# Kernel tuning notes

Hardware: AMD Instinct MI355X
Metric: run time of the kernel (lower is better)

## Reference

```python
import jax, jax.numpy as jnp
import numpy as np

N, E, D, ED, G = 50000, 800000, 64, 32, 50


def setup_inputs() -> dict:
    key = jax.random.key(0)
    ks = jax.random.split(key, 24)
    s = 0.05
    inp = {
        "x": jax.random.normal(ks[0], (N, D), jnp.float32),
        "edge_attr": jax.random.normal(ks[1], (E, ED), jnp.float32),
        "edge_index": jax.random.randint(ks[2], (2, E), 0, N, jnp.int64),
    }
    i = 3
    for step in range(2):
        inp[f"fe{step}_W1"] = jax.random.normal(ks[i], (2 * D + ED, D), jnp.float32) * s; i += 1
        inp[f"fe{step}_b1"] = jnp.zeros((D,), jnp.float32)
        inp[f"fe{step}_W2"] = jax.random.normal(ks[i], (D, D), jnp.float32) * s; i += 1
        inp[f"fe{step}_b2"] = jnp.zeros((D,), jnp.float32)
        inp[f"lstm{step}_Wih"] = jax.random.normal(ks[i], (D, 4 * D), jnp.float32) * s; i += 1
        inp[f"lstm{step}_Whh"] = jax.random.normal(ks[i], (D, 4 * D), jnp.float32) * s; i += 1
        inp[f"lstm{step}_bih"] = jnp.zeros((4 * D,), jnp.float32)
        inp[f"lstm{step}_bhh"] = jnp.zeros((4 * D,), jnp.float32)
    inp["gm_W"] = jax.random.normal(ks[i], (D, G), jnp.float32) * s; i += 1
    inp["gm_b"] = jnp.zeros((G,), jnp.float32)
    inp["fm_W"] = jax.random.normal(ks[i], (D, G), jnp.float32) * s; i += 1
    inp["fm_b"] = jnp.zeros((G,), jnp.float32)
    return inp


def _mpn(x, edge_attr, src, dst, W1, b1, W2, b2):
    # x_i = x[dst] (target), x_j = x[src] (source); aggregate 'add' at dst
    m = jnp.concatenate([x[dst], x[src], edge_attr], axis=1)  # [E, 2D+ED]
    m = jax.nn.relu(m @ W1 + b1) @ W2 + b2                    # [E, D]
    return jax.ops.segment_sum(m, dst, num_segments=x.shape[0])


def _lstm_cell(inp, h, c, Wih, Whh, bih, bhh):
    gates = inp @ Wih + h @ Whh + (bih + bhh)  # [N, 4D], gate order i,f,g,o
    i, f, g, o = jnp.split(gates, 4, axis=1)
    c = jax.nn.sigmoid(f) * c + jax.nn.sigmoid(i) * jnp.tanh(g)
    h = jax.nn.sigmoid(o) * jnp.tanh(c)
    return h, c


def reference(x, edge_attr, edge_index,
              fe0_W1, fe0_b1, fe0_W2, fe0_b2,
              lstm0_Wih, lstm0_Whh, lstm0_bih, lstm0_bhh,
              fe1_W1, fe1_b1, fe1_W2, fe1_b2,
              lstm1_Wih, lstm1_Whh, lstm1_bih, lstm1_bhh,
              gm_W, gm_b, fm_W, fm_b):
    src, dst = edge_index[0], edge_index[1]
    c = jnp.zeros_like(x)
    fes = [(fe0_W1, fe0_b1, fe0_W2, fe0_b2), (fe1_W1, fe1_b1, fe1_W2, fe1_b2)]
    lstms = [(lstm0_Wih, lstm0_Whh, lstm0_bih, lstm0_bhh),
             (lstm1_Wih, lstm1_Whh, lstm1_bih, lstm1_bhh)]
    for step in range(2):
        a = _mpn(x, edge_attr, src, dst, *fes[step])
        # LSTMCell(input=x, (h=a, c=c)) as in the original forward
        x, c = _lstm_cell(x, a, c, *lstms[step])
    g = jax.nn.sigmoid(x @ gm_W + gm_b)   # [N, G]
    h_v_G = x @ fm_W + fm_b               # [N, G]
    return jnp.sum(g * h_v_G, axis=0)     # [G]
```

## Files before the change

### kernel.cpp

```cpp
#include <hip/hip_runtime.h>
#include <hip/hip_bf16.h>

using short8 = __attribute__((ext_vector_type(8))) short;
using f32x4  = __attribute__((ext_vector_type(4))) float;

#define K1P 168
#define KLP 136

__device__ __forceinline__ unsigned short f2bf(float f) {
  unsigned u = __float_as_uint(f);
  u += 0x7FFFu + ((u >> 16) & 1u);
  return (unsigned short)(u >> 16);
}
__device__ __forceinline__ unsigned pack2(float a, float b) {
  return (unsigned)f2bf(a) | ((unsigned)f2bf(b) << 16);
}
#if __has_builtin(__builtin_amdgcn_rcpf)
__device__ __forceinline__ float fast_rcp(float x) { return __builtin_amdgcn_rcpf(x); }
#else
__device__ __forceinline__ float fast_rcp(float x) { return 1.f / x; }
#endif
__device__ __forceinline__ float sigm(float x) { return fast_rcp(1.f + __expf(-x)); }
__device__ __forceinline__ float tanh_f(float x) { return fmaf(2.f, sigm(2.f * x), -1.f); }

__global__ __launch_bounds__(256) void prep_simple(
    const float* __restrict__ W1_0, const float* __restrict__ Wih0,
    const float* __restrict__ bih0, const float* __restrict__ bhh0,
    const float* __restrict__ W1_1, const float* __restrict__ Wih1,
    const float* __restrict__ bih1, const float* __restrict__ bhh1,
    const float* __restrict__ gmW, const float* __restrict__ fmW,
    unsigned short* __restrict__ W1T,
    unsigned short* __restrict__ WcT,
    float* __restrict__ bG,
    unsigned short* __restrict__ WrT)
{
  int t = blockIdx.x * 256 + threadIdx.x;
  const int per = 10240 + 16384 + 256;
  if (t >= 2 * per + 8192) return;
  if (t >= 2 * per) {
    int r2 = t - 2 * per;
    int o = r2 >> 6, k = r2 & 63;
    float v = 0.f;
    if (o < 50) v = gmW[k * 50 + o];
    else if (o >= 64 && o < 114) v = fmW[k * 50 + (o - 64)];
    WrT[o * 64 + k] = f2bf(v);
    return;
  }
  int step = t / per, r = t % per;
  const float* W1  = step ? W1_1 : W1_0;
  const float* Wih = step ? Wih1 : Wih0;
  const float* bih = step ? bih1 : bih0;
  const float* bhh = step ? bhh1 : bhh0;
  if (r < 10240) {
    int o = r / 160, k = r % 160;
    W1T[step * 10240 + o * 160 + k] = f2bf(W1[k * 64 + o]);
  } else if (r < 26624) {
    int rr = r - 10240;
    int g = rr >> 6, k = rr & 63;
    WcT[step * 32768 + g * 128 + k] = f2bf(Wih[k * 256 + g]);
  } else {
    int g = r - 26624;
    bG[step * 256 + g] = bih[g] + bhh[g];
  }
}

__global__ __launch_bounds__(256) void prep_merge(
    const float* __restrict__ W2_0, const float* __restrict__ Whh0, const float* __restrict__ b2_0,
    const float* __restrict__ W2_1, const float* __restrict__ Whh1, const float* __restrict__ b2_1,
    unsigned short* __restrict__ WcT,
    float* __restrict__ b2h)
{
  int t = blockIdx.x * 256 + threadIdx.x;
  if (t < 32768) {
    int step = t >> 14, r = t & 16383;
    int g = r >> 6, k = r & 63;
    const float* W2  = step ? W2_1 : W2_0;
    const float* Whh = step ? Whh1 : Whh0;
    float v = 0.f;
    for (int j = 0; j < 64; ++j) v = fmaf(W2[k * 64 + j], Whh[j * 256 + g], v);
    WcT[step * 32768 + g * 128 + 64 + k] = f2bf(v);
  } else if (t < 33280) {
    int r = t - 32768;
    int step = r >> 8, g = r & 255;
    const float* b2  = step ? b2_1 : b2_0;
    const float* Whh = step ? Whh1 : Whh0;
    float v = 0.f;
    for (int j = 0; j < 64; ++j) v = fmaf(b2[j], Whh[j * 256 + g], v);
    b2h[step * 256 + g] = v;
  }
}

__global__ __launch_bounds__(256) void convert_x(
    const float* __restrict__ x, unsigned short* __restrict__ xb, int n)
{
  int i = blockIdx.x * 256 + threadIdx.x;
  if (i < n) xb[i] = f2bf(x[i]);
}

__global__ __launch_bounds__(256) void hist_kernel(
    const int* __restrict__ dstI, int* __restrict__ hist, int E)
{
  int e = blockIdx.x * 256 + threadIdx.x;
  if (e < E) atomicAdd(&hist[dstI[e]], 1);
}

__global__ __launch_bounds__(256) void scan_part(
    const int* __restrict__ hist, int2* __restrict__ blockTot, int N)
{
  __shared__ int sD[256], sS[256];
  int t = threadIdx.x;
  int n = blockIdx.x * 256 + t;
  int d = (n < N) ? hist[n] : 0;
  int sg = (d + 15) >> 4;
  sD[t] = d; sS[t] = sg;
  __syncthreads();
  #pragma unroll
  for (int off = 128; off; off >>= 1) {
    if (t < off) { sD[t] += sD[t + off]; sS[t] += sS[t + off]; }
    __syncthreads();
  }
  if (t == 0) blockTot[blockIdx.x] = make_int2(sD[0], sS[0]);
}

__global__ __launch_bounds__(256) void scan_mid(
    const int2* __restrict__ blockTot, int2* __restrict__ blockBase,
    int* __restrict__ nSegTot, int nb)
{
  __shared__ int sD[256], sS[256];
  int t = threadIdx.x;
  int d = 0, s = 0;
  if (t < nb) { int2 v = blockTot[t]; d = v.x; s = v.y; }
  sD[t] = d; sS[t] = s;
  __syncthreads();
  #pragma unroll
  for (int off = 1; off < 256; off <<= 1) {
    int vd = (t >= off) ? sD[t - off] : 0;
    int vs = (t >= off) ? sS[t - off] : 0;
    __syncthreads();
    sD[t] += vd; sS[t] += vs;
    __syncthreads();
  }
  if (t < nb) blockBase[t] = make_int2(sD[t] - d, sS[t] - s);
  if (t == nb - 1) *nSegTot = sS[t];
}

__global__ __launch_bounds__(256) void scan_final(
    const int* __restrict__ hist, const int2* __restrict__ blockBase,
    int* __restrict__ cursor, int4* __restrict__ segInfo, int N)
{
  __shared__ int sD[256], sS[256];
  int t = threadIdx.x;
  int n = blockIdx.x * 256 + t;
  int d = (n < N) ? hist[n] : 0;
  int sg = (d + 15) >> 4;
  sD[t] = d; sS[t] = sg;
  __syncthreads();
  #pragma unroll
  for (int off = 1; off < 256; off <<= 1) {
    int vd = (t >= off) ? sD[t - off] : 0;
    int vs = (t >= off) ? sS[t - off] : 0;
    __syncthreads();
    sD[t] += vd; sS[t] += vs;
    __syncthreads();
  }
  if (n < N) {
    int2 bb = blockBase[blockIdx.x];
    int degBase = bb.x + sD[t] - d;
    int segBase = bb.y + sS[t] - sg;
    cursor[n] = degBase;
    for (int j = 0; j < sg; ++j)
      segInfo[segBase + j] = make_int4(degBase + j * 16, n, min(d - j * 16, 16), 0);
  }
}

__global__ __launch_bounds__(256) void scatter_perm(
    const int* __restrict__ srcI, const int* __restrict__ dstI,
    const float* __restrict__ ea, int* __restrict__ cursor,
    int* __restrict__ srcS, unsigned short* __restrict__ eaS, int E)
{
  int e = blockIdx.x * 256 + threadIdx.x;
  if (e >= E) return;
  int d = dstI[e];
  int p = atomicAdd(&cursor[d], 1);
  srcS[p] = srcI[e];
  const float4* pe = (const float4*)(ea + (long long)e * 32);
  float4 a0 = pe[0], a1 = pe[1], a2 = pe[2], a3 = pe[3];
  float4 a4 = pe[4], a5 = pe[5], a6 = pe[6], a7 = pe[7];
  uint4* out = (uint4*)(eaS + (long long)p * 32);
  out[0] = make_uint4(pack2(a0.x, a0.y), pack2(a0.z, a0.w), pack2(a1.x, a1.y), pack2(a1.z, a1.w));
  out[1] = make_uint4(pack2(a2.x, a2.y), pack2(a2.z, a2.w), pack2(a3.x, a3.y), pack2(a3.z, a3.w));
  out[2] = make_uint4(pack2(a4.x, a4.y), pack2(a4.z, a4.w), pack2(a5.x, a5.y), pack2(a5.z, a5.w));
  out[3] = make_uint4(pack2(a6.x, a6.y), pack2(a6.z, a6.w), pack2(a7.x, a7.y), pack2(a7.z, a7.w));
}

__global__ __launch_bounds__(256) void edge_gemm_agg(
    const unsigned short* __restrict__ xb,
    const unsigned short* __restrict__ eaS,
    const int* __restrict__ srcS,
    const int4* __restrict__ segInfo,
    const int* __restrict__ nSegPtr,
    const unsigned short* __restrict__ W1T,
    const float* __restrict__ b1,
    float* __restrict__ aggrH)
{
  __shared__ unsigned short sM[64 * K1P];
  __shared__ unsigned short sW1[64 * 21 * 8];
  __shared__ float sB1[64];
  const int t = threadIdx.x;
  {
    const uint4* gw1 = (const uint4*)W1T;
    uint4* lw1 = (uint4*)sW1;
    #pragma unroll
    for (int p = 0; p < 5; ++p) {
      int idx = t + p * 256;
      int o = idx / 20, s = idx % 20;
      lw1[o * 21 + s] = gw1[idx];
    }
    if (t < 64) sB1[t] = b1[t];
  }
  __syncthreads();

  const int w = t >> 6, l = t & 63;
  const int quad = l >> 4, lr = l & 15;
  const int r = l >> 2, q = l & 3;
  unsigned short* rowp = sM + (w * 16 + r) * K1P;
  const int nSeg = *nSegPtr;
  const int W = gridDim.x * 4;

  for (int s = blockIdx.x * 4 + w; s < nSeg; s += W) {
    int4 si = segInfo[s];
    const int start = si.x, node = si.y, cnt = si.z;

    const uint4* pd = (const uint4*)(xb + (long long)node * 64);
    *(uint4*)(rowp + q * 16)     = pd[q * 2];
    *(uint4*)(rowp + q * 16 + 8) = pd[q * 2 + 1];
    int src = (r < cnt) ? srcS[start + r] : 0;
    const uint4* ps = (const uint4*)(xb + (long long)src * 64);
    *(uint4*)(rowp + 64 + q * 16)     = ps[q * 2];
    *(uint4*)(rowp + 64 + q * 16 + 8) = ps[q * 2 + 1];
    const uint4* pe = (const uint4*)(eaS + (long long)(start + r) * 32);
    *(uint4*)(rowp + 128 + q * 8) = pe[q];

    f32x4 acc[4] = {};
    #pragma unroll
    for (int kc = 0; kc < 5; ++kc) {
      short8 aF = *(const short8*)(sM + (w * 16 + lr) * K1P + kc * 32 + quad * 8);
      #pragma unroll
      for (int n = 0; n < 4; ++n) {
        short8 bF = *(const short8*)(sW1 + (n * 16 + lr) * K1P + kc * 32 + quad * 8);
        acc[n] = __builtin_amdgcn_mfma_f32_16x16x32_bf16(aF, bF, acc[n], 0, 0, 0);
      }
    }

    #pragma unroll
    for (int n = 0; n < 4; ++n) {
      int col = n * 16 + lr;
      float bb = sB1[col];
      float sum = 0.f;
      #pragma unroll
      for (int rr = 0; rr < 4; ++rr) {
        int rowi = quad * 4 + rr;
        float v = fmaxf(acc[n][rr] + bb, 0.f);
        sum += (rowi < cnt) ? v : 0.f;
      }
      sum += __shfl_xor(sum, 16);
      sum += __shfl_xor(sum, 32);
      if (quad == 0) unsafeAtomicAdd(&aggrH[(long long)node * 64 + col], sum);
    }
  }
}

__global__ __launch_bounds__(256) void lstm3(
    const float* __restrict__ xin,
    const float* __restrict__ aggrH,
    const float* __restrict__ cin,
    float* __restrict__ cout,
    const unsigned short* __restrict__ WcT,
    const float* __restrict__ bG,
    const float* __restrict__ b2h,
    const int* __restrict__ degA,
    float* __restrict__ xout,
    unsigned short* __restrict__ xbf_out,
    int nNodes)
{
  __shared__ unsigned short sIn[64 * KLP];
  __shared__ unsigned short sW[64 * KLP];
  __shared__ float sBG[256], sB2h[256];
  const int t = threadIdx.x;
  sBG[t] = bG[t];
  sB2h[t] = b2h[t];

  const int base_n = blockIdx.x * 64;
  const int nl = t >> 2, q = t & 3;
  const int node = base_n + nl;
  unsigned short* rowp = sIn + nl * KLP;
  if (node < nNodes) {
    const float4* px = (const float4*)(xin + (long long)node * 64) + q * 4;
    float4 v0 = px[0], v1 = px[1], v2 = px[2], v3 = px[3];
    *(uint4*)(rowp + q * 16) =
        make_uint4(pack2(v0.x, v0.y), pack2(v0.z, v0.w), pack2(v1.x, v1.y), pack2(v1.z, v1.w));
    *(uint4*)(rowp + q * 16 + 8) =
        make_uint4(pack2(v2.x, v2.y), pack2(v2.z, v2.w), pack2(v3.x, v3.y), pack2(v3.z, v3.w));
    const float4* pg = (const float4*)(aggrH + (long long)node * 64) + q * 4;
    float4 g0 = pg[0], g1 = pg[1], g2 = pg[2], g3 = pg[3];
    *(uint4*)(rowp + 64 + q * 16) =
        make_uint4(pack2(g0.x, g0.y), pack2(g0.z, g0.w), pack2(g1.x, g1.y), pack2(g1.z, g1.w));
    *(uint4*)(rowp + 64 + q * 16 + 8) =
        make_uint4(pack2(g2.x, g2.y), pack2(g2.z, g2.w), pack2(g3.x, g3.y), pack2(g3.z, g3.w));
  } else {
    *(uint4*)(rowp + q * 16)          = make_uint4(0, 0, 0, 0);
    *(uint4*)(rowp + q * 16 + 8)      = make_uint4(0, 0, 0, 0);
    *(uint4*)(rowp + 64 + q * 16)     = make_uint4(0, 0, 0, 0);
    *(uint4*)(rowp + 64 + q * 16 + 8) = make_uint4(0, 0, 0, 0);
  }

  const int w = t >> 6, l = t & 63, quad = l >> 4, lr = l & 15;
  const int row0 = w * 16;
  f32x4 acc[16] = {};
  for (int grp = 0; grp < 4; ++grp) {
    const uint4* gw = (const uint4*)WcT + (long long)(grp * 64) * 16;
    uint4* lw = (uint4*)sW;
    {
      int o0 = t >> 4, s4 = t & 15;
      #pragma unroll
      for (int p = 0; p < 4; ++p) {
        int o = p * 16 + o0;
        lw[o * 17 + s4] = gw[o * 16 + s4];
      }
    }
    __syncthreads();
    #pragma unroll
    for (int kc = 0; kc < 4; ++kc) {
      short8 aF = *(const short8*)(sIn + (row0 + lr) * KLP + kc * 32 + quad * 8);
      #pragma unroll
      for (int nt = 0; nt < 4; ++nt) {
        short8 bF = *(const short8*)(sW + (nt * 16 + lr) * KLP + kc * 32 + quad * 8);
        acc[grp * 4 + nt] = __builtin_amdgcn_mfma_f32_16x16x32_bf16(aF, bF, acc[grp * 4 + nt], 0, 0, 0);
      }
    }
    __syncthreads();
  }

  #pragma unroll
  for (int nt = 0; nt < 4; ++nt) {
    #pragma unroll
    for (int rr = 0; rr < 4; ++rr) {
      int node2 = base_n + row0 + quad * 4 + rr;
      if (node2 < nNodes) {
        int col = nt * 16 + lr;
        long long off = (long long)node2 * 64 + col;
        float dg = (float)degA[node2];
        float iv = acc[nt][rr]      + sBG[col]       + dg * sB2h[col];
        float fv = acc[4 + nt][rr]  + sBG[64 + col]  + dg * sB2h[64 + col];
        float gv = acc[8 + nt][rr]  + sBG[128 + col] + dg * sB2h[128 + col];
        float ov = acc[12 + nt][rr] + sBG[192 + col] + dg * sB2h[192 + col];
        float cOld = cin ? cin[off] : 0.f;
        float cN = sigm(fv) * cOld + sigm(iv) * tanh_f(gv);
        float hN = sigm(ov) * tanh_f(cN);
        cout[off] = cN;
        xout[off] = hN;
        if (xbf_out) xbf_out[off] = f2bf(hN);
      }
    }
  }
}

__global__ __launch_bounds__(256) void readout(
    const float* __restrict__ x,
    const unsigned short* __restrict__ WrT,
    const float* __restrict__ gb, const float* __restrict__ fb,
    float* __restrict__ out, int nNodes)
{
  __shared__ unsigned short sX[64 * 72];
  __shared__ unsigned short sW[128 * 72];
  __shared__ float sOut[4][64];
  __shared__ float sGb[64], sFb[64];
  const int t = threadIdx.x;
  {
    const uint4* gw = (const uint4*)WrT;
    uint4* lw = (uint4*)sW;
    #pragma unroll
    for (int p = 0; p < 4; ++p) {
      int idx = t + p * 256;
      int o = idx >> 3, s = idx & 7;
      lw[o * 9 + s] = gw[idx];
    }
    if (t < 50)      { sGb[t] = gb[t]; sFb[t] = fb[t]; }
    else if (t < 64) { sGb[t] = 0.f;   sFb[t] = 0.f; }
  }
  const int base = blockIdx.x * 64;
  const int nl = t >> 2, q = t & 3;
  const int node = base + nl;
  {
    uint2* dst = (uint2*)(sX + nl * 72 + q * 16);
    if (node < nNodes) {
      const float4* px = (const float4*)(x + (long long)node * 64) + q * 4;
      #pragma unroll
      for (int j = 0; j < 4; ++j) {
        float4 v = px[j];
        dst[j] = make_uint2(pack2(v.x, v.y), pack2(v.z, v.w));
      }
    } else {
      #pragma unroll
      for (int j = 0; j < 4; ++j) dst[j] = make_uint2(0, 0);
    }
  }
  __syncthreads();

  const int w = t >> 6, l = t & 63, quad = l >> 4, lr = l & 15;
  f32x4 acc[8] = {};
  #pragma unroll
  for (int kc = 0; kc < 2; ++kc) {
    short8 aF = *(const short8*)(sX + (w * 16 + lr) * 72 + kc * 32 + quad * 8);
    #pragma unroll
    for (int n = 0; n < 8; ++n) {
      short8 bF = *(const short8*)(sW + (n * 16 + lr) * 72 + kc * 32 + quad * 8);
      acc[n] = __builtin_amdgcn_mfma_f32_16x16x32_bf16(aF, bF, acc[n], 0, 0, 0);
    }
  }
  #pragma unroll
  for (int n = 0; n < 4; ++n) {
    float val = 0.f;
    #pragma unroll
    for (int rr = 0; rr < 4; ++rr) {
      int nd = base + w * 16 + quad * 4 + rr;
      if (nd < nNodes) {
        int jj = n * 16 + lr;
        float gv = sigm(acc[n][rr] + sGb[jj]);
        float fv = acc[n + 4][rr] + sFb[jj];
        val += gv * fv;
      }
    }
    val += __shfl_xor(val, 16);
    val += __shfl_xor(val, 32);
    if (quad == 0) sOut[w][n * 16 + lr] = val;
  }
  __syncthreads();
  if (t < 50) {
    float s = sOut[0][t] + sOut[1][t] + sOut[2][t] + sOut[3][t];
    unsafeAtomicAdd(&out[t], s);
  }
}

extern "C" void kernel_launch(void* const* d_in, const int* in_sizes, int n_in,
                              void* d_out, int out_size, void* d_ws, size_t ws_size,
                              hipStream_t stream)
{
  const float* x      = (const float*)d_in[0];
  const float* ea     = (const float*)d_in[1];
  const int*   ei     = (const int*)d_in[2];
  const float* fe0_W1 = (const float*)d_in[3];
  const float* fe0_b1 = (const float*)d_in[4];
  const float* fe0_W2 = (const float*)d_in[5];
  const float* fe0_b2 = (const float*)d_in[6];
  const float* l0_Wih = (const float*)d_in[7];
  const float* l0_Whh = (const float*)d_in[8];
  const float* l0_bih = (const float*)d_in[9];
  const float* l0_bhh = (const float*)d_in[10];
  const float* fe1_W1 = (const float*)d_in[11];
  const float* fe1_b1 = (const float*)d_in[12];
  const float* fe1_W2 = (const float*)d_in[13];
  const float* fe1_b2 = (const float*)d_in[14];
  const float* l1_Wih = (const float*)d_in[15];
  const float* l1_Whh = (const float*)d_in[16];
  const float* l1_bih = (const float*)d_in[17];
  const float* l1_bhh = (const float*)d_in[18];
  const float* gm_W   = (const float*)d_in[19];
  const float* gm_b   = (const float*)d_in[20];
  const float* fm_W   = (const float*)d_in[21];
  const float* fm_b   = (const float*)d_in[22];

  const int N = in_sizes[0] / 64;
  const int E = in_sizes[1] / 32;
  const int* srcI = ei;
  const int* dstI = ei + E;

  char* ws = (char*)d_ws;
  unsigned short* xb      = (unsigned short*)(ws + 0);
  float*          x1      = (float*)(ws + 6400000);
  float*          aggrH   = (float*)(ws + 19200000);
  float*          cbuf    = (float*)(ws + 32000000);
  unsigned short* eaS     = (unsigned short*)(ws + 44800000);
  int*            srcS    = (int*)(ws + 96001024);
  int4*           segInfo = (int4*)(ws + 99201088);
  int*            histA   = (int*)(ws + 100801216);
  int*            curA    = (int*)(ws + 101001216);
  unsigned short* W1T     = (unsigned short*)(ws + 101201216);
  unsigned short* WcT     = (unsigned short*)(ws + 101242176);
  float*          bG      = (float*)(ws + 101373248);
  float*          b2h     = (float*)(ws + 101375296);
  unsigned short* WrT     = (unsigned short*)(ws + 101377344);
  int*            nSegPtr = (int*)(ws + 101393728);
  int2*           blockTot  = (int2*)(ws + 101393792);
  int2*           blockBase = (int2*)(ws + 101395840);

  hipMemsetAsync(d_out, 0, out_size * sizeof(float), stream);
  hipMemsetAsync(histA, 0, (size_t)N * 4, stream);

  prep_simple<<<(2 * 26880 + 8192 + 255) / 256, 256, 0, stream>>>(
      fe0_W1, l0_Wih, l0_bih, l0_bhh,
      fe1_W1, l1_Wih, l1_bih, l1_bhh,
      gm_W, fm_W, W1T, WcT, bG, WrT);
  prep_merge<<<(33280 + 255) / 256, 256, 0, stream>>>(
      fe0_W2, l0_Whh, fe0_b2, fe1_W2, l1_Whh, fe1_b2, WcT, b2h);
  convert_x<<<(N * 64 + 255) / 256, 256, 0, stream>>>(x, xb, N * 64);

  const int nb = (N + 255) / 256;
  hist_kernel<<<(E + 255) / 256, 256, 0, stream>>>(dstI, histA, E);
  scan_part<<<nb, 256, 0, stream>>>(histA, blockTot, N);
  scan_mid<<<1, 256, 0, stream>>>(blockTot, blockBase, nSegPtr, nb);
  scan_final<<<nb, 256, 0, stream>>>(histA, blockBase, curA, segInfo, N);
  scatter_perm<<<(E + 255) / 256, 256, 0, stream>>>(srcI, dstI, ea, curA, srcS, eaS, E);

  const int nodeBlocks = (N + 63) / 64;

  hipMemsetAsync(aggrH, 0, (size_t)N * 64 * 4, stream);
  edge_gemm_agg<<<768, 256, 0, stream>>>(xb, eaS, srcS, segInfo, nSegPtr,
                                         W1T, fe0_b1, aggrH);
  lstm3<<<nodeBlocks, 256, 0, stream>>>(x, aggrH, nullptr, cbuf, WcT, bG, b2h,
                                        histA, x1, xb, N);

  hipMemsetAsync(aggrH, 0, (size_t)N * 64 * 4, stream);
  edge_gemm_agg<<<768, 256, 0, stream>>>(xb, eaS, srcS, segInfo, nSegPtr,
                                         W1T + 10240, fe1_b1, aggrH);
  lstm3<<<nodeBlocks, 256, 0, stream>>>(x1, aggrH, cbuf, cbuf, WcT + 32768,
                                        bG + 256, b2h + 256, histA, x1, nullptr, N);

  readout<<<nodeBlocks, 256, 0, stream>>>(x1, WrT, gm_b, fm_b, (float*)d_out, N);
}
```

Baseline: 490.9 us.

## Register-resident edge GEMM, split scatter into eid scatter plus gather, bf16 node states

The edge GEMM kernel now keeps the W1 fragments in registers and loads A fragments straight from global memory, removing the LDS staging and the block barrier. It uses a 3-waves occupancy hint and a larger grid. The edge permutation is split into an atomic scatter of edge ids followed by a coalesced-write gather of src and edge_attr. Node states between steps are stored only in bf16 (ping-pong xb0/xb1), so the fp32 x copies disappear and lstm and readout read half the bytes. The costs are register pressure in the edge kernel, an extra kernel launch, and the LSTM input x now rounded to bf16, which it already was before the MFMA.

```diff
diff --git a/kernel.cpp b/kernel.cpp
--- a/kernel.cpp
+++ b/kernel.cpp
@@ -4,7 +4,6 @@
 using short8 = __attribute__((ext_vector_type(8))) short;
 using f32x4  = __attribute__((ext_vector_type(4))) float;
 
-#define K1P 168
 #define KLP 136
 
 __device__ __forceinline__ unsigned short f2bf(float f) {
@@ -173,17 +172,27 @@
   }
 }
 
-__global__ __launch_bounds__(256) void scatter_perm(
-    const int* __restrict__ srcI, const int* __restrict__ dstI,
-    const float* __restrict__ ea, int* __restrict__ cursor,
-    int* __restrict__ srcS, unsigned short* __restrict__ eaS, int E)
+__global__ __launch_bounds__(256) void scatter_eid(
+    const int* __restrict__ dstI, int* __restrict__ cursor,
+    int* __restrict__ eidS, int E)
 {
   int e = blockIdx.x * 256 + threadIdx.x;
   if (e >= E) return;
   int d = dstI[e];
   int p = atomicAdd(&cursor[d], 1);
-  srcS[p] = srcI[e];
-  const float4* pe = (const float4*)(ea + (long long)e * 32);
+  eidS[p] = e;
+}
+
+__global__ __launch_bounds__(256) void gather_perm(
+    const int* __restrict__ eidS, const int* __restrict__ srcI,
+    const float* __restrict__ ea,
+    int* __restrict__ srcS, unsigned short* __restrict__ eaS, int E)
+{
+  int p = blockIdx.x * 256 + threadIdx.x;
+  if (p >= E) return;
+  int eid = eidS[p];
+  srcS[p] = srcI[eid];
+  const float4* pe = (const float4*)(ea + (long long)eid * 32);
   float4 a0 = pe[0], a1 = pe[1], a2 = pe[2], a3 = pe[3];
   float4 a4 = pe[4], a5 = pe[5], a6 = pe[6], a7 = pe[7];
   uint4* out = (uint4*)(eaS + (long long)p * 32);
@@ -193,7 +202,7 @@
   out[3] = make_uint4(pack2(a6.x, a6.y), pack2(a6.z, a6.w), pack2(a7.x, a7.y), pack2(a7.z, a7.w));
 }
 
-__global__ __launch_bounds__(256) void edge_gemm_agg(
+__global__ __launch_bounds__(256, 3) void edge_gemm_reg(
     const unsigned short* __restrict__ xb,
     const unsigned short* __restrict__ eaS,
     const int* __restrict__ srcS,
@@ -203,75 +212,67 @@
     const float* __restrict__ b1,
     float* __restrict__ aggrH)
 {
-  __shared__ unsigned short sM[64 * K1P];
-  __shared__ unsigned short sW1[64 * 21 * 8];
-  __shared__ float sB1[64];
   const int t = threadIdx.x;
-  {
-    const uint4* gw1 = (const uint4*)W1T;
-    uint4* lw1 = (uint4*)sW1;
-    #pragma unroll
-    for (int p = 0; p < 5; ++p) {
-      int idx = t + p * 256;
-      int o = idx / 20, s = idx % 20;
-      lw1[o * 21 + s] = gw1[idx];
-    }
-    if (t < 64) sB1[t] = b1[t];
-  }
-  __syncthreads();
-
   const int w = t >> 6, l = t & 63;
   const int quad = l >> 4, lr = l & 15;
-  const int r = l >> 2, q = l & 3;
-  unsigned short* rowp = sM + (w * 16 + r) * K1P;
+
+  short8 bF[5][4];
+  #pragma unroll
+  for (int kc = 0; kc < 5; ++kc)
+    #pragma unroll
+    for (int n = 0; n < 4; ++n)
+      bF[kc][n] = *(const short8*)(W1T + (n * 16 + lr) * 160 + kc * 32 + quad * 8);
+  float bb[4];
+  #pragma unroll
+  for (int n = 0; n < 4; ++n) bb[n] = b1[n * 16 + lr];
+
   const int nSeg = *nSegPtr;
   const int W = gridDim.x * 4;
 
   for (int s = blockIdx.x * 4 + w; s < nSeg; s += W) {
     int4 si = segInfo[s];
     const int start = si.x, node = si.y, cnt = si.z;
-
-    const uint4* pd = (const uint4*)(xb + (long long)node * 64);
-    *(uint4*)(rowp + q * 16)     = pd[q * 2];
-    *(uint4*)(rowp + q * 16 + 8) = pd[q * 2 + 1];
-    int src = (r < cnt) ? srcS[start + r] : 0;
-    const uint4* ps = (const uint4*)(xb + (long long)src * 64);
-    *(uint4*)(rowp + 64 + q * 16)     = ps[q * 2];
-    *(uint4*)(rowp + 64 + q * 16 + 8) = ps[q * 2 + 1];
-    const uint4* pe = (const uint4*)(eaS + (long long)(start + r) * 32);
-    *(uint4*)(rowp + 128 + q * 8) = pe[q];
+    const int er = min(lr, cnt - 1);
+    const int src = srcS[start + er];
+
+    const short8* pd = (const short8*)(xb + (long long)node * 64);
+    const short8* ps = (const short8*)(xb + (long long)src * 64);
+    const short8* pe = (const short8*)(eaS + (long long)(start + er) * 32);
+    short8 a0 = pd[quad];
+    short8 a1 = pd[4 + quad];
+    short8 a2 = ps[quad];
+    short8 a3 = ps[4 + quad];
+    short8 a4 = pe[quad];
 
     f32x4 acc[4] = {};
     #pragma unroll
-    for (int kc = 0; kc < 5; ++kc) {
-      short8 aF = *(const short8*)(sM + (w * 16 + lr) * K1P + kc * 32 + quad * 8);
-      #pragma unroll
-      for (int n = 0; n < 4; ++n) {
-        short8 bF = *(const short8*)(sW1 + (n * 16 + lr) * K1P + kc * 32 + quad * 8);
-        acc[n] = __builtin_amdgcn_mfma_f32_16x16x32_bf16(aF, bF, acc[n], 0, 0, 0);
-      }
-    }
+    for (int n = 0; n < 4; ++n) acc[n] = __builtin_amdgcn_mfma_f32_16x16x32_bf16(a0, bF[0][n], acc[n], 0, 0, 0);
+    #pragma unroll
+    for (int n = 0; n < 4; ++n) acc[n] = __builtin_amdgcn_mfma_f32_16x16x32_bf16(a1, bF[1][n], acc[n], 0, 0, 0);
+    #pragma unroll
+    for (int n = 0; n < 4; ++n) acc[n] = __builtin_amdgcn_mfma_f32_16x16x32_bf16(a2, bF[2][n], acc[n], 0, 0, 0);
+    #pragma unroll
+    for (int n = 0; n < 4; ++n) acc[n] = __builtin_amdgcn_mfma_f32_16x16x32_bf16(a3, bF[3][n], acc[n], 0, 0, 0);
+    #pragma unroll
+    for (int n = 0; n < 4; ++n) acc[n] = __builtin_amdgcn_mfma_f32_16x16x32_bf16(a4, bF[4][n], acc[n], 0, 0, 0);
 
     #pragma unroll
     for (int n = 0; n < 4; ++n) {
-      int col = n * 16 + lr;
-      float bb = sB1[col];
       float sum = 0.f;
       #pragma unroll
       for (int rr = 0; rr < 4; ++rr) {
-        int rowi = quad * 4 + rr;
-        float v = fmaxf(acc[n][rr] + bb, 0.f);
-        sum += (rowi < cnt) ? v : 0.f;
+        float v = fmaxf(acc[n][rr] + bb[n], 0.f);
+        sum += (quad * 4 + rr < cnt) ? v : 0.f;
       }
       sum += __shfl_xor(sum, 16);
       sum += __shfl_xor(sum, 32);
-      if (quad == 0) unsafeAtomicAdd(&aggrH[(long long)node * 64 + col], sum);
+      if (quad == 0) unsafeAtomicAdd(&aggrH[(long long)node * 64 + n * 16 + lr], sum);
     }
   }
 }
 
 __global__ __launch_bounds__(256) void lstm3(
-    const float* __restrict__ xin,
+    const unsigned short* __restrict__ xbin,
     const float* __restrict__ aggrH,
     const float* __restrict__ cin,
     float* __restrict__ cout,
@@ -279,8 +280,7 @@
     const float* __restrict__ bG,
     const float* __restrict__ b2h,
     const int* __restrict__ degA,
-    float* __restrict__ xout,
-    unsigned short* __restrict__ xbf_out,
+    unsigned short* __restrict__ xbout,
     int nNodes)
 {
   __shared__ unsigned short sIn[64 * KLP];
@@ -295,12 +295,9 @@
   const int node = base_n + nl;
   unsigned short* rowp = sIn + nl * KLP;
   if (node < nNodes) {
-    const float4* px = (const float4*)(xin + (long long)node * 64) + q * 4;
-    float4 v0 = px[0], v1 = px[1], v2 = px[2], v3 = px[3];
-    *(uint4*)(rowp + q * 16) =
-        make_uint4(pack2(v0.x, v0.y), pack2(v0.z, v0.w), pack2(v1.x, v1.y), pack2(v1.z, v1.w));
-    *(uint4*)(rowp + q * 16 + 8) =
-        make_uint4(pack2(v2.x, v2.y), pack2(v2.z, v2.w), pack2(v3.x, v3.y), pack2(v3.z, v3.w));
+    const uint4* px = (const uint4*)(xbin + (long long)node * 64);
+    *(uint4*)(rowp + q * 16)     = px[q * 2];
+    *(uint4*)(rowp + q * 16 + 8) = px[q * 2 + 1];
     const float4* pg = (const float4*)(aggrH + (long long)node * 64) + q * 4;
     float4 g0 = pg[0], g1 = pg[1], g2 = pg[2], g3 = pg[3];
     *(uint4*)(rowp + 64 + q * 16) =
@@ -358,15 +355,14 @@
         float cN = sigm(fv) * cOld + sigm(iv) * tanh_f(gv);
         float hN = sigm(ov) * tanh_f(cN);
         cout[off] = cN;
-        xout[off] = hN;
-        if (xbf_out) xbf_out[off] = f2bf(hN);
+        xbout[off] = f2bf(hN);
       }
     }
   }
 }
 
 __global__ __launch_bounds__(256) void readout(
-    const float* __restrict__ x,
+    const unsigned short* __restrict__ xq,
     const unsigned short* __restrict__ WrT,
     const float* __restrict__ gb, const float* __restrict__ fb,
     float* __restrict__ out, int nNodes)
@@ -392,17 +388,14 @@
   const int nl = t >> 2, q = t & 3;
   const int node = base + nl;
   {
-    uint2* dst = (uint2*)(sX + nl * 72 + q * 16);
+    uint4* dst = (uint4*)(sX + nl * 72 + q * 16);
     if (node < nNodes) {
-      const float4* px = (const float4*)(x + (long long)node * 64) + q * 4;
-      #pragma unroll
-      for (int j = 0; j < 4; ++j) {
-        float4 v = px[j];
-        dst[j] = make_uint2(pack2(v.x, v.y), pack2(v.z, v.w));
-      }
+      const uint4* px = (const uint4*)(xq + (long long)node * 64);
+      dst[0] = px[q * 2];
+      dst[1] = px[q * 2 + 1];
     } else {
-      #pragma unroll
-      for (int j = 0; j < 4; ++j) dst[j] = make_uint2(0, 0);
+      dst[0] = make_uint4(0, 0, 0, 0);
+      dst[1] = make_uint4(0, 0, 0, 0);
     }
   }
   __syncthreads();
@@ -476,23 +469,24 @@
   const int* dstI = ei + E;
 
   char* ws = (char*)d_ws;
-  unsigned short* xb      = (unsigned short*)(ws + 0);
-  float*          x1      = (float*)(ws + 6400000);
-  float*          aggrH   = (float*)(ws + 19200000);
-  float*          cbuf    = (float*)(ws + 32000000);
-  unsigned short* eaS     = (unsigned short*)(ws + 44800000);
-  int*            srcS    = (int*)(ws + 96001024);
-  int4*           segInfo = (int4*)(ws + 99201088);
-  int*            histA   = (int*)(ws + 100801216);
-  int*            curA    = (int*)(ws + 101001216);
-  unsigned short* W1T     = (unsigned short*)(ws + 101201216);
-  unsigned short* WcT     = (unsigned short*)(ws + 101242176);
-  float*          bG      = (float*)(ws + 101373248);
-  float*          b2h     = (float*)(ws + 101375296);
-  unsigned short* WrT     = (unsigned short*)(ws + 101377344);
-  int*            nSegPtr = (int*)(ws + 101393728);
-  int2*           blockTot  = (int2*)(ws + 101393792);
-  int2*           blockBase = (int2*)(ws + 101395840);
+  unsigned short* xb0     = (unsigned short*)(ws + 0);
+  unsigned short* xb1     = (unsigned short*)(ws + 6400000);
+  float*          aggrH   = (float*)(ws + 12800000);
+  float*          cbuf    = (float*)(ws + 25600000);
+  unsigned short* eaS     = (unsigned short*)(ws + 38400000);
+  int*            eidS    = (int*)(ws + 89601024);
+  int*            srcS    = (int*)(ws + 92801088);
+  int4*           segInfo = (int4*)(ws + 96001152);
+  int*            histA   = (int*)(ws + 97601280);
+  int*            curA    = (int*)(ws + 97801280);
+  unsigned short* W1T     = (unsigned short*)(ws + 98001280);
+  unsigned short* WcT     = (unsigned short*)(ws + 98042240);
+  float*          bG      = (float*)(ws + 98173312);
+  float*          b2h     = (float*)(ws + 98175360);
+  unsigned short* WrT     = (unsigned short*)(ws + 98177408);
+  int*            nSegPtr = (int*)(ws + 98193792);
+  int2*           blockTot  = (int2*)(ws + 98193856);
+  int2*           blockBase = (int2*)(ws + 98195904);
 
   hipMemsetAsync(d_out, 0, out_size * sizeof(float), stream);
   hipMemsetAsync(histA, 0, (size_t)N * 4, stream);
@@ -503,28 +497,29 @@
       gm_W, fm_W, W1T, WcT, bG, WrT);
   prep_merge<<<(33280 + 255) / 256, 256, 0, stream>>>(
       fe0_W2, l0_Whh, fe0_b2, fe1_W2, l1_Whh, fe1_b2, WcT, b2h);
-  convert_x<<<(N * 64 + 255) / 256, 256, 0, stream>>>(x, xb, N * 64);
+  convert_x<<<(N * 64 + 255) / 256, 256, 0, stream>>>(x, xb0, N * 64);
 
   const int nb = (N + 255) / 256;
   hist_kernel<<<(E + 255) / 256, 256, 0, stream>>>(dstI, histA, E);
   scan_part<<<nb, 256, 0, stream>>>(histA, blockTot, N);
   scan_mid<<<1, 256, 0, stream>>>(blockTot, blockBase, nSegPtr, nb);
   scan_final<<<nb, 256, 0, stream>>>(histA, blockBase, curA, segInfo, N);
-  scatter_perm<<<(E + 255) / 256, 256, 0, stream>>>(srcI, dstI, ea, curA, srcS, eaS, E);
+  scatter_eid<<<(E + 255) / 256, 256, 0, stream>>>(dstI, curA, eidS, E);
+  gather_perm<<<(E + 255) / 256, 256, 0, stream>>>(eidS, srcI, ea, srcS, eaS, E);
 
   const int nodeBlocks = (N + 63) / 64;
 
   hipMemsetAsync(aggrH, 0, (size_t)N * 64 * 4, stream);
-  edge_gemm_agg<<<768, 256, 0, stream>>>(xb, eaS, srcS, segInfo, nSegPtr,
-                                         W1T, fe0_b1, aggrH);
-  lstm3<<<nodeBlocks, 256, 0, stream>>>(x, aggrH, nullptr, cbuf, WcT, bG, b2h,
-                                        histA, x1, xb, N);
+  edge_gemm_reg<<<1024, 256, 0, stream>>>(xb0, eaS, srcS, segInfo, nSegPtr,
+                                          W1T, fe0_b1, aggrH);
+  lstm3<<<nodeBlocks, 256, 0, stream>>>(xb0, aggrH, nullptr, cbuf, WcT, bG, b2h,
+                                        histA, xb1, N);
 
   hipMemsetAsync(aggrH, 0, (size_t)N * 64 * 4, stream);
-  edge_gemm_agg<<<768, 256, 0, stream>>>(xb, eaS, srcS, segInfo, nSegPtr,
-                                         W1T + 10240, fe1_b1, aggrH);
-  lstm3<<<nodeBlocks, 256, 0, stream>>>(x1, aggrH, cbuf, cbuf, WcT + 32768,
-                                        bG + 256, b2h + 256, histA, x1, nullptr, N);
-
-  readout<<<nodeBlocks, 256, 0, stream>>>(x1, WrT, gm_b, fm_b, (float*)d_out, N);
-}
+  edge_gemm_reg<<<1024, 256, 0, stream>>>(xb1, eaS, srcS, segInfo, nSegPtr,
+                                          W1T + 10240, fe1_b1, aggrH);
+  lstm3<<<nodeBlocks, 256, 0, stream>>>(xb1, aggrH, cbuf, cbuf, WcT + 32768,
+                                        bG + 256, b2h + 256, histA, xb0, N);
+
+  readout<<<nodeBlocks, 256, 0, stream>>>(xb0, WrT, gm_b, fm_b, (float*)d_out, N);
+}
```

Measured after the change: 561.4 us. 14.4% more time.
